# Optimization experiments

Measured on AMD Instinct MI355X. Metric: run time of the kernel, lower is better.

## Reference

```python
import jax, jax.numpy as jnp
import numpy as np

NUM_EXPERTS = 8
NUM_ROWS = 1024
HIDDEN = 2048
INTER = 1024
TOPK = 2


def setup_inputs() -> dict:
    key = jax.random.key(0)
    kx, kr, k1, k2, k3 = jax.random.split(key, 5)
    x = jax.random.normal(kx, (NUM_ROWS, HIDDEN), dtype=jnp.float32)
    router_probs = jax.random.normal(kr, (NUM_ROWS, NUM_EXPERTS), dtype=jnp.float32)
    fc1 = jax.random.uniform(k1, (NUM_EXPERTS, HIDDEN, INTER), minval=-0.1, maxval=0.1, dtype=jnp.float32)
    fc2 = jax.random.uniform(k2, (NUM_EXPERTS, INTER, HIDDEN), minval=-0.1, maxval=0.1, dtype=jnp.float32)
    fc3 = jax.random.uniform(k3, (NUM_EXPERTS, HIDDEN, INTER), minval=-0.1, maxval=0.1, dtype=jnp.float32)
    return {"x": x, "router_probs": router_probs, "fc1": fc1, "fc2": fc2, "fc3": fc3}


def reference(x, router_probs, fc1, fc2, fc3):
    # Router: softmax over experts, top-k, renormalize
    router_softmax = jax.nn.softmax(router_probs.astype(jnp.float32), axis=1).astype(router_probs.dtype)
    topk_probs, topk_indices = jax.lax.top_k(router_softmax, TOPK)  # [N,K]
    topk_probs = topk_probs / jnp.sum(topk_probs, axis=1, keepdims=True)

    # Per-token combine weight for each expert: w[n,e] = sum_k prob[n,k]*[idx[n,k]==e]
    one_hot = jax.nn.one_hot(topk_indices, NUM_EXPERTS, dtype=x.dtype)  # [N,K,E]
    combine = jnp.einsum("nk,nke->ne", topk_probs, one_hot)  # [N,E]

    # Dense grouped GEMMs over all experts (reference form of dispatch/combine)
    h1 = jnp.einsum("nh,ehi->eni", x, fc1)  # [E,N,I]
    h3 = jnp.einsum("nh,ehi->eni", x, fc3)  # [E,N,I]
    act = jax.nn.silu(h1) * h3  # swiglu
    h2 = jnp.einsum("eni,eih->enh", act, fc2)  # [E,N,H]
    out = jnp.einsum("ne,enh->nh", combine, h2)  # [N,H]
    return out
```

## Files before the change

kernel.cpp:

```cpp
#include <hip/hip_runtime.h>

#define NEXP 8
#define NTOK 1024
#define HID 2048
#define ITR 1024

typedef __attribute__((ext_vector_type(8))) short short8;
typedef __attribute__((ext_vector_type(4))) short short4v;
typedef __attribute__((ext_vector_type(4))) float f32x4;
typedef __attribute__((ext_vector_type(2))) float f32x2;
typedef __attribute__((ext_vector_type(2))) unsigned uint2v;

__device__ __forceinline__ unsigned short f2bf(float f) {
  unsigned u = __float_as_uint(f);
  u += 0x7fffu + ((u >> 16) & 1u);
  return (unsigned short)(u >> 16);
}

__device__ __forceinline__ void gl_lds16(const void* g, void* l) {
  __builtin_amdgcn_global_load_lds(
      (const __attribute__((address_space(1))) unsigned int*)g,
      (__attribute__((address_space(3))) unsigned int*)l, 16, 0, 0);
}

__global__ __launch_bounds__(256) void k_setup(const float* __restrict__ x,
                                               unsigned int* __restrict__ xb,
                                               float* __restrict__ out) {
  int i = blockIdx.x * 256 + threadIdx.x;
  f32x4 z = {0.f, 0.f, 0.f, 0.f};
  *(f32x4*)(out + (size_t)i * 4) = z;
  f32x4 v = *(const f32x4*)(x + (size_t)i * 4);
  xb[(size_t)i * 2] = (unsigned)f2bf(v[0]) | ((unsigned)f2bf(v[1]) << 16);
  xb[(size_t)i * 2 + 1] = (unsigned)f2bf(v[2]) | ((unsigned)f2bf(v[3]) << 16);
}

__global__ __launch_bounds__(1024) void k_router(const float* __restrict__ rp,
                                                 int* __restrict__ counts,
                                                 int* __restrict__ base,
                                                 int* __restrict__ toklist,
                                                 float* __restrict__ wlist) {
  __shared__ int c[NEXP];
  __shared__ int sb[NEXP];
  int n = threadIdx.x;
  if (n < NEXP) c[n] = 0;
  __syncthreads();
  float r[NEXP];
#pragma unroll
  for (int e = 0; e < NEXP; ++e) r[e] = rp[n * NEXP + e];
  int i1 = 0;
  float m1 = r[0];
#pragma unroll
  for (int e = 1; e < NEXP; ++e)
    if (r[e] > m1) { m1 = r[e]; i1 = e; }
  int i2 = -1;
  float m2 = -3.4e38f;
#pragma unroll
  for (int e = 0; e < NEXP; ++e)
    if (e != i1 && r[e] > m2) { m2 = r[e]; i2 = e; }
  float p1 = 1.f / (1.f + __expf(m2 - m1));
  float p2 = 1.f - p1;
  int s1 = atomicAdd(&c[i1], 1);
  int s2 = atomicAdd(&c[i2], 1);
  __syncthreads();
  if (n == 0) {
    int a = 0;
#pragma unroll
    for (int e = 0; e < NEXP; ++e) { sb[e] = a; a += c[e]; }
  }
  __syncthreads();
  int q1 = sb[i1] + s1;
  toklist[q1] = n; wlist[q1] = p1;
  int q2 = sb[i2] + s2;
  toklist[q2] = n; wlist[q2] = p2;
  if (n < NEXP) { counts[n] = c[n]; base[n] = sb[n]; }
}

__global__ __launch_bounds__(512, 4) void k_gemm13(
    const float* __restrict__ fc1, const float* __restrict__ fc3,
    const unsigned short* __restrict__ xb, const int* __restrict__ counts,
    const int* __restrict__ base, const int* __restrict__ toklist,
    unsigned short* __restrict__ act) {
  const int bid = blockIdx.x;
  const int e = bid & 7;
  const int t2 = bid >> 3;
  const int ntile = t2 & 31;
  const int mtile = t2 >> 5;
  const int cnt = counts[e];
  const int mbase = mtile * 256;
  if (mbase >= cnt) return;
  const int n0t = ntile * 32;
  const int rbase = base[e];

  __shared__ __align__(16) unsigned short lds[2 * 20480];
  const int tid = threadIdx.x;
  const int lane = tid & 63, w = tid >> 6;

  const unsigned short* srcA[4];
  int dofA[4];
#pragma unroll
  for (int i = 0; i < 4; ++i) {
    int cc = i * 512 + tid;
    int r = cc >> 3, b = cc & 7;
    int row = mbase + r;
    int tok = toklist[rbase + ((row < cnt) ? row : (cnt - 1))];
    srcA[i] = xb + (size_t)tok * HID + (b ^ (r & 7)) * 8;
    dofA[i] = (i * 512 + w * 64) * 8;
  }

  const int mat = tid >> 8;
  const int c8 = tid & 255;
  const int kq = c8 >> 4;
  const int n0 = (c8 & 15) * 2;
  const float* wsrc = (mat ? fc3 : fc1) + (size_t)e * HID * ITR +
                      (size_t)(kq * 4) * ITR + n0t + n0;
  int wrb[2];
#pragma unroll
  for (int t = 0; t < 2; ++t) {
    int nn = n0 + t;
    wrb[t] = 32768 + mat * 4096 + nn * 128 + ((kq ^ (nn & 15)) << 3);
  }

  int offA[2][2], woff[2][2][2];
#pragma unroll
  for (int mi = 0; mi < 2; ++mi)
#pragma unroll
    for (int s = 0; s < 2; ++s) {
      int kb = s * 4 + (lane >> 4);
      int rowA = w * 32 + mi * 16 + (lane & 15);
      offA[mi][s] = rowA * 128 + ((kb ^ (rowA & 7)) << 4);
    }
#pragma unroll
  for (int ni = 0; ni < 2; ++ni)
#pragma unroll
    for (int s = 0; s < 2; ++s) {
      int n = ni * 16 + (lane & 15);
      int kb0 = s * 8 + (lane >> 4) * 2;
      woff[ni][s][0] = n * 128 + ((kb0 ^ (n & 15)) << 3);
      woff[ni][s][1] = n * 128 + (((kb0 + 1) ^ (n & 15)) << 3);
    }

  f32x4 acc1[2][2], acc3[2][2];
#pragma unroll
  for (int mi = 0; mi < 2; ++mi)
#pragma unroll
    for (int ni = 0; ni < 2; ++ni) {
      acc1[mi][ni] = (f32x4){0.f, 0.f, 0.f, 0.f};
      acc3[mi][ni] = (f32x4){0.f, 0.f, 0.f, 0.f};
    }

  float wvA[8], wvB[8];

#define STGA13(bb, kt)                                    \
  {                                                       \
    int k0 = (kt) * 64;                                   \
    unsigned short* Lb = lds + (bb) * 20480;              \
    _Pragma("unroll") for (int i = 0; i < 4; ++i)         \
        gl_lds16(srcA[i] + k0, Lb + dofA[i]);             \
  }
#define LOADW13(wv, kt)                                   \
  {                                                       \
    const float* g = wsrc + (size_t)(kt) * 64 * ITR;      \
    _Pragma("unroll") for (int j = 0; j < 4; ++j) {       \
      f32x2 vv = *(const f32x2*)(g + (size_t)j * ITR);    \
      wv[2 * j] = vv[0];                                  \
      wv[2 * j + 1] = vv[1];                              \
    }                                                     \
  }
#define CVTW13(wv, bb)                                                        \
  {                                                                           \
    _Pragma("unroll") for (int t = 0; t < 2; ++t) {                           \
      unsigned lo = (unsigned)f2bf(wv[t]) | ((unsigned)f2bf(wv[2 + t]) << 16);\
      unsigned hi =                                                           \
          (unsigned)f2bf(wv[4 + t]) | ((unsigned)f2bf(wv[6 + t]) << 16);      \
      uint2v v = {lo, hi};                                                    \
      *(uint2v*)((char*)lds + (bb) * 40960 + wrb[t]) = v;                     \
    }                                                                         \
  }
#define COMPUTE13(bb)                                                         \
  {                                                                           \
    const char* Lb = (const char*)lds + (bb) * 40960;                         \
    _Pragma("unroll") for (int s = 0; s < 2; ++s) {                           \
      short8 af[2];                                                           \
      _Pragma("unroll") for (int mi = 0; mi < 2; ++mi)                        \
          af[mi] = *(const short8*)(Lb + offA[mi][s]);                        \
      _Pragma("unroll") for (int ni = 0; ni < 2; ++ni) {                      \
        short4v l1 = *(const short4v*)(Lb + 32768 + woff[ni][s][0]);          \
        short4v h1 = *(const short4v*)(Lb + 32768 + woff[ni][s][1]);          \
        short4v l3 = *(const short4v*)(Lb + 36864 + woff[ni][s][0]);          \
        short4v h3 = *(const short4v*)(Lb + 36864 + woff[ni][s][1]);          \
        short8 w1f = __builtin_shufflevector(l1, h1, 0, 1, 2, 3, 4, 5, 6, 7); \
        short8 w3f = __builtin_shufflevector(l3, h3, 0, 1, 2, 3, 4, 5, 6, 7); \
        _Pragma("unroll") for (int mi = 0; mi < 2; ++mi) {                    \
          acc1[mi][ni] = __builtin_amdgcn_mfma_f32_16x16x32_bf16(             \
              af[mi], w1f, acc1[mi][ni], 0, 0, 0);                            \
          acc3[mi][ni] = __builtin_amdgcn_mfma_f32_16x16x32_bf16(             \
              af[mi], w3f, acc3[mi][ni], 0, 0, 0);                            \
        }                                                                     \
      }                                                                       \
    }                                                                         \
  }

  LOADW13(wvA, 0);
  STGA13(0, 0);
  CVTW13(wvA, 0);
  LOADW13(wvB, 1);
  __syncthreads();
  for (int kt = 0; kt < 32; kt += 2) {
    STGA13(1, kt + 1);
    CVTW13(wvB, 1);
    if (kt + 2 < 32) LOADW13(wvA, kt + 2);
    COMPUTE13(0);
    __syncthreads();
    if (kt + 2 < 32) {
      STGA13(0, kt + 2);
      CVTW13(wvA, 0);
    }
    if (kt + 3 < 32) LOADW13(wvB, kt + 3);
    COMPUTE13(1);
    __syncthreads();
  }

  unsigned short* lact = lds;
#pragma unroll
  for (int mi = 0; mi < 2; ++mi)
#pragma unroll
    for (int ni = 0; ni < 2; ++ni)
#pragma unroll
      for (int rr = 0; rr < 4; ++rr) {
        float h1 = acc1[mi][ni][rr], h3 = acc3[mi][ni][rr];
        float a = h1 * (1.f / (1.f + __expf(-h1))) * h3;
        int row = w * 32 + mi * 16 + (lane >> 4) * 4 + rr;
        int col = ni * 16 + (lane & 15);
        lact[row * 40 + col] = f2bf(a);
      }
  __syncthreads();
#pragma unroll
  for (int p = 0; p < 2; ++p) {
    int row = p * 128 + (tid >> 2);
    int q = (tid & 3) * 8;
    if (mbase + row < cnt)
      *(short8*)(act + (size_t)(rbase + mbase + row) * ITR + n0t + q) =
          *(const short8*)&lact[row * 40 + q];
  }
}

__global__ __launch_bounds__(512, 4) void k_gemm2(
    const float* __restrict__ fc2, const unsigned short* __restrict__ act,
    const int* __restrict__ counts, const int* __restrict__ base,
    const int* __restrict__ toklist, const float* __restrict__ wlist,
    float* __restrict__ out) {
  const int bid = blockIdx.x;
  const int e = bid & 7;
  const int t2 = bid >> 3;
  const int ntile = t2 & 63;
  const int mtile = t2 >> 6;
  const int cnt = counts[e];
  const int mbase = mtile * 256;
  if (mbase >= cnt) return;
  const int n0t = ntile * 32;
  const int rbase = base[e];

  __shared__ __align__(16) unsigned short lds[2 * 18432];
  const int tid = threadIdx.x;
  const int lane = tid & 63, w = tid >> 6;

  const unsigned short* srcA[4];
  int dofA[4];
#pragma unroll
  for (int i = 0; i < 4; ++i) {
    int cc = i * 512 + tid;
    int r = cc >> 3, b = cc & 7;
    int arow = rbase + mbase + r;
    if (arow > 2047) arow = 2047;
    srcA[i] = act + (size_t)arow * ITR + (b ^ (r & 7)) * 8;
    dofA[i] = (i * 512 + w * 64) * 8;
  }

  const int kq = tid >> 5;
  const int n0 = tid & 31;
  const float* wsrc =
      fc2 + (size_t)e * ITR * HID + (size_t)(kq * 4) * HID + n0t + n0;
  const int wrb = 32768 + n0 * 128 + ((kq ^ (n0 & 15)) << 3);

  int offA[2][2], woff[2][2][2];
#pragma unroll
  for (int mi = 0; mi < 2; ++mi)
#pragma unroll
    for (int s = 0; s < 2; ++s) {
      int kb = s * 4 + (lane >> 4);
      int rowA = w * 32 + mi * 16 + (lane & 15);
      offA[mi][s] = rowA * 128 + ((kb ^ (rowA & 7)) << 4);
    }
#pragma unroll
  for (int ni = 0; ni < 2; ++ni)
#pragma unroll
    for (int s = 0; s < 2; ++s) {
      int n = ni * 16 + (lane & 15);
      int kb0 = s * 8 + (lane >> 4) * 2;
      woff[ni][s][0] = n * 128 + ((kb0 ^ (n & 15)) << 3);
      woff[ni][s][1] = n * 128 + (((kb0 + 1) ^ (n & 15)) << 3);
    }

  f32x4 acc[2][2];
#pragma unroll
  for (int mi = 0; mi < 2; ++mi)
#pragma unroll
    for (int ni = 0; ni < 2; ++ni) acc[mi][ni] = (f32x4){0.f, 0.f, 0.f, 0.f};

  float wvA[4], wvB[4];

#define STGA2(bb, kt)                                     \
  {                                                       \
    int k0 = (kt) * 64;                                   \
    unsigned short* Lb = lds + (bb) * 18432;              \
    _Pragma("unroll") for (int i = 0; i < 4; ++i)         \
        gl_lds16(srcA[i] + k0, Lb + dofA[i]);             \
  }
#define LOADW2(wv, kt)                                    \
  {                                                       \
    const float* g = wsrc + (size_t)(kt) * 64 * HID;      \
    _Pragma("unroll") for (int j = 0; j < 4; ++j)         \
        wv[j] = g[(size_t)j * HID];                       \
  }
#define CVTW2(wv, bb)                                                       \
  {                                                                         \
    unsigned lo = (unsigned)f2bf(wv[0]) | ((unsigned)f2bf(wv[1]) << 16);    \
    unsigned hi = (unsigned)f2bf(wv[2]) | ((unsigned)f2bf(wv[3]) << 16);    \
    uint2v v = {lo, hi};                                                    \
    *(uint2v*)((char*)lds + (bb) * 36864 + wrb) = v;                        \
  }
#define COMPUTE2(bb)                                                          \
  {                                                                           \
    const char* Lb = (const char*)lds + (bb) * 36864;                         \
    _Pragma("unroll") for (int s = 0; s < 2; ++s) {                           \
      short8 af[2];                                                           \
      _Pragma("unroll") for (int mi = 0; mi < 2; ++mi)                        \
          af[mi] = *(const short8*)(Lb + offA[mi][s]);                        \
      _Pragma("unroll") for (int ni = 0; ni < 2; ++ni) {                      \
        short4v lw = *(const short4v*)(Lb + 32768 + woff[ni][s][0]);          \
        short4v hw = *(const short4v*)(Lb + 32768 + woff[ni][s][1]);          \
        short8 wf = __builtin_shufflevector(lw, hw, 0, 1, 2, 3, 4, 5, 6, 7);  \
        _Pragma("unroll") for (int mi = 0; mi < 2; ++mi)                      \
            acc[mi][ni] = __builtin_amdgcn_mfma_f32_16x16x32_bf16(            \
                af[mi], wf, acc[mi][ni], 0, 0, 0);                            \
      }                                                                       \
    }                                                                         \
  }

  LOADW2(wvA, 0);
  STGA2(0, 0);
  CVTW2(wvA, 0);
  LOADW2(wvB, 1);
  __syncthreads();
  for (int kt = 0; kt < 16; kt += 2) {
    STGA2(1, kt + 1);
    CVTW2(wvB, 1);
    if (kt + 2 < 16) LOADW2(wvA, kt + 2);
    COMPUTE2(0);
    __syncthreads();
    if (kt + 2 < 16) {
      STGA2(0, kt + 2);
      CVTW2(wvA, 0);
    }
    if (kt + 3 < 16) LOADW2(wvB, kt + 3);
    COMPUTE2(1);
    __syncthreads();
  }

#pragma unroll
  for (int mi = 0; mi < 2; ++mi)
#pragma unroll
    for (int rr = 0; rr < 4; ++rr) {
      int lr = w * 32 + mi * 16 + (lane >> 4) * 4 + rr;
      int grow = mbase + lr;
      if (grow < cnt) {
        float pv = wlist[rbase + grow];
        int tok = toklist[rbase + grow];
        float* orow = out + (size_t)tok * HID + n0t + (lane & 15);
#pragma unroll
        for (int ni = 0; ni < 2; ++ni)
          atomicAdd(orow + ni * 16, acc[mi][ni][rr] * pv);
      }
    }
}

extern "C" void kernel_launch(void* const* d_in, const int* in_sizes, int n_in,
                              void* d_out, int out_size, void* d_ws,
                              size_t ws_size, hipStream_t stream) {
  (void)in_sizes; (void)n_in; (void)out_size; (void)ws_size;
  const float* x = (const float*)d_in[0];
  const float* rp = (const float*)d_in[1];
  const float* fc1 = (const float*)d_in[2];
  const float* fc2 = (const float*)d_in[3];
  const float* fc3 = (const float*)d_in[4];
  float* out = (float*)d_out;
  char* ws = (char*)d_ws;

  int* counts = (int*)ws;
  int* base = (int*)(ws + 256);
  int* toklist = (int*)(ws + 4096);
  float* wlist = (float*)(ws + 12288);
  unsigned short* xb = (unsigned short*)(ws + 32768);
  unsigned short* act = (unsigned short*)(ws + 4227072);

  k_setup<<<2048, 256, 0, stream>>>(x, (unsigned int*)xb, out);
  k_router<<<1, 1024, 0, stream>>>(rp, counts, base, toklist, wlist);
  k_gemm13<<<1024, 512, 0, stream>>>(fc1, fc3, xb, counts, base, toklist, act);
  k_gemm2<<<2048, 512, 0, stream>>>(fc2, act, counts, base, toklist, wlist, out);
}
```

Baseline: 282.6 us.

## Restructure GEMM k-loop pipeline with explicit vmcnt waits and raw barriers

Both grouped-GEMM main loops are reorganised so the weight register prefetch and the A-tile global-to-LDS copy are issued together, each followed by a partial s_waitcnt vmcnt(8) instead of a full drain. __syncthreads is replaced with s_barrier plus sched_barrier fences. Tail iterations clamp to the last tile index instead of branching. The aim is to keep more global loads in flight across the conversion and compute phases. In exchange it adds a barrier per half-step, redundant loads on the tail, and depends on the hard-coded vmcnt count matching the number of issued loads.

```diff
diff --git a/kernel.cpp b/kernel.cpp
--- a/kernel.cpp
+++ b/kernel.cpp
@@ -22,6 +22,22 @@
       (const __attribute__((address_space(1))) unsigned int*)g,
       (__attribute__((address_space(3))) unsigned int*)l, 16, 0, 0);
 }
+
+#define VMCNT8                                           \
+  do {                                                   \
+    asm volatile("s_waitcnt vmcnt(8)" ::: "memory");     \
+    __builtin_amdgcn_sched_barrier(0);                   \
+  } while (0)
+#define LGKM0                                            \
+  do {                                                   \
+    asm volatile("s_waitcnt lgkmcnt(0)" ::: "memory");   \
+    __builtin_amdgcn_sched_barrier(0);                   \
+  } while (0)
+#define BARRIER                                          \
+  do {                                                   \
+    __builtin_amdgcn_s_barrier();                        \
+    __builtin_amdgcn_sched_barrier(0);                   \
+  } while (0)
 
 __global__ __launch_bounds__(256) void k_setup(const float* __restrict__ x,
                                                unsigned int* __restrict__ xb,
@@ -201,23 +217,38 @@
   }
 
   LOADW13(wvA, 0);
+  LOADW13(wvB, 1);
   STGA13(0, 0);
+  VMCNT8;
   CVTW13(wvA, 0);
-  LOADW13(wvB, 1);
-  __syncthreads();
+  LGKM0;
+  BARRIER;
+
   for (int kt = 0; kt < 32; kt += 2) {
-    STGA13(1, kt + 1);
-    CVTW13(wvB, 1);
-    if (kt + 2 < 32) LOADW13(wvA, kt + 2);
-    COMPUTE13(0);
-    __syncthreads();
-    if (kt + 2 < 32) {
-      STGA13(0, kt + 2);
+    {
+      int kw = kt + 2 < 32 ? kt + 2 : 31;
+      int ka = kt + 1 < 32 ? kt + 1 : 31;
+      LOADW13(wvA, kw);
+      STGA13(1, ka);
+      VMCNT8;
+      CVTW13(wvB, 1);
+      LGKM0;
+      BARRIER;
+      COMPUTE13(0);
+      BARRIER;
+    }
+    {
+      int kw = kt + 3 < 32 ? kt + 3 : 31;
+      int ka = kt + 2 < 32 ? kt + 2 : 31;
+      LOADW13(wvB, kw);
+      STGA13(0, ka);
+      VMCNT8;
       CVTW13(wvA, 0);
-    }
-    if (kt + 3 < 32) LOADW13(wvB, kt + 3);
-    COMPUTE13(1);
-    __syncthreads();
+      LGKM0;
+      BARRIER;
+      COMPUTE13(1);
+      BARRIER;
+    }
   }
 
   unsigned short* lact = lds;
@@ -348,23 +379,38 @@
   }
 
   LOADW2(wvA, 0);
+  LOADW2(wvB, 1);
   STGA2(0, 0);
+  VMCNT8;
   CVTW2(wvA, 0);
-  LOADW2(wvB, 1);
-  __syncthreads();
+  LGKM0;
+  BARRIER;
+
   for (int kt = 0; kt < 16; kt += 2) {
-    STGA2(1, kt + 1);
-    CVTW2(wvB, 1);
-    if (kt + 2 < 16) LOADW2(wvA, kt + 2);
-    COMPUTE2(0);
-    __syncthreads();
-    if (kt + 2 < 16) {
-      STGA2(0, kt + 2);
+    {
+      int kw = kt + 2 < 16 ? kt + 2 : 15;
+      int ka = kt + 1 < 16 ? kt + 1 : 15;
+      LOADW2(wvA, kw);
+      STGA2(1, ka);
+      VMCNT8;
+      CVTW2(wvB, 1);
+      LGKM0;
+      BARRIER;
+      COMPUTE2(0);
+      BARRIER;
+    }
+    {
+      int kw = kt + 3 < 16 ? kt + 3 : 15;
+      int ka = kt + 2 < 16 ? kt + 2 : 15;
+      LOADW2(wvB, kw);
+      STGA2(0, ka);
+      VMCNT8;
       CVTW2(wvA, 0);
-    }
-    if (kt + 3 < 16) LOADW2(wvB, kt + 3);
-    COMPUTE2(1);
-    __syncthreads();
+      LGKM0;
+      BARRIER;
+      COMPUTE2(1);
+      BARRIER;
+    }
   }
 
 #pragma unroll
```

Measured after the change: 299.7 us. 6.0% more time.
